# Kernel optimization log

Hardware: AMD Instinct MI355X
Metric: run time of the kernel (lower is better)

The kernel has to match this reference:

```python
import jax, jax.numpy as jnp
import numpy as np
import math

B, L, DF = 1024, 96, 5
D_MODEL, D_FF, N_HEADS = 256, 1024, 8
C_OUT, MA, FACTOR = 5, 25, 3
E_LAYERS, D_LAYERS, EXT = 2, 2, 20


def moving_mean(x, k):
    # torch moving_avg: replicate-pad (k-1)//2 on each side, AvgPool1d(k, stride=1)
    p = (k - 1) // 2
    xp = jnp.concatenate([jnp.repeat(x[:, :1], p, axis=1), x, jnp.repeat(x[:, -1:], p, axis=1)], axis=1)
    cs = jnp.cumsum(xp, axis=1)
    cs = jnp.concatenate([jnp.zeros_like(cs[:, :1]), cs], axis=1)
    return (cs[:, k:] - cs[:, :-k]) / k


def series_decomp(x, k):
    m = moving_mean(x, k)
    return x - m, m


def circ_conv3(x, W):
    # Conv1d(kernel=3, padding=1, padding_mode='circular', bias=False); x (B,T,C), W (O,C,3)
    xp = jnp.pad(x, ((0, 0), (1, 1), (0, 0)), mode='wrap')
    win = jnp.stack([xp[:, :-2], xp[:, 1:-1], xp[:, 2:]], axis=-1)  # (B,T,C,3)
    return jnp.einsum('btct,oct->bto'.replace('btct', 'blct').replace('bto', 'blo'), win, W)


def my_layernorm(x, g, b):
    # LayerNorm over last dim, then subtract per-(batch,channel) seasonal bias (mean over time)
    mu = x.mean(-1, keepdims=True)
    var = ((x - mu) ** 2).mean(-1, keepdims=True)
    xh = (x - mu) / jnp.sqrt(var + 1e-5) * g + b
    return xh - xh.mean(axis=1, keepdims=True)


def time_delay_agg(values, corr):
    # inference-mode time delay aggregation; values, corr: (B,H,E,Lv)
    Bv, H, E, Lv = values.shape
    top_k = int(FACTOR * math.log(Lv))
    mean_value = corr.mean(axis=(1, 2))              # (B,Lv)
    weights, delay = jax.lax.top_k(mean_value, top_k)  # (B,k)
    tmp_corr = jax.nn.softmax(weights, axis=-1)
    ar = jnp.arange(Lv)

    def body(acc, wd):
        w, d = wd                                    # (B,), (B,) int32
        idx = (ar[None, :] + d[:, None]) % Lv        # circular roll == gather on doubled values
        pattern = jnp.take_along_axis(values, idx[:, None, None, :], axis=-1)
        return acc + pattern * w[:, None, None, None], None

    acc, _ = jax.lax.scan(body, jnp.zeros_like(values), (tmp_corr.T, delay.T))
    return acc


def auto_correlation(q, k, v):
    # q (B,Lq,H,E); k,v (B,S,H,E)
    Bq, Lq, H, E = q.shape
    S = v.shape[1]
    if Lq > S:
        pad = jnp.zeros((Bq, Lq - S, H, E), q.dtype)
        k = jnp.concatenate([k, pad], axis=1)
        v = jnp.concatenate([v, pad], axis=1)
    else:
        k, v = k[:, :Lq], v[:, :Lq]
    qf = jnp.fft.rfft(q.transpose(0, 2, 3, 1), axis=-1)
    kf = jnp.fft.rfft(k.transpose(0, 2, 3, 1), axis=-1)
    corr = jnp.fft.irfft(qf * jnp.conj(kf), n=Lq, axis=-1)  # (B,H,E,Lq)
    V = time_delay_agg(v.transpose(0, 2, 3, 1), corr)
    return V.transpose(0, 3, 1, 2)


def ac_layer(xq, xkv, Wq, bq, Wk, bk, Wv, bv, Wo, bo):
    Bq, Lq, _ = xq.shape
    S = xkv.shape[1]
    q = (xq @ Wq.T + bq).reshape(Bq, Lq, N_HEADS, -1)
    k = (xkv @ Wk.T + bk).reshape(Bq, S, N_HEADS, -1)
    v = (xkv @ Wv.T + bv).reshape(Bq, S, N_HEADS, -1)
    V = auto_correlation(q, k, v).reshape(Bq, Lq, -1)
    return V @ Wo.T + bo


def setup_inputs() -> dict:
    ks = iter(jax.random.split(jax.random.key(0), 64))

    def rn(shape, s=0.05):
        return jax.random.normal(next(ks), shape, jnp.float32) * s

    dm, E, D = D_MODEL, E_LAYERS, D_LAYERS
    inp = {'x': jax.random.normal(next(ks), (B, L, DF), jnp.float32)}
    inp['we_enc'] = rn((dm, DF, 3), 0.3)
    inp['we_dec'] = rn((dm, DF, 3), 0.3)
    for w in ('Wq', 'Wk', 'Wv', 'Wo'):
        inp['enc_' + w] = rn((E, dm, dm))
        inp['enc_b' + w[1]] = rn((E, dm))
    inp['enc_W1'] = rn((E, D_FF, dm))
    inp['enc_W2'] = rn((E, dm, D_FF))
    inp['enc_ln_g'] = jnp.ones((dm,), jnp.float32)
    inp['enc_ln_b'] = jnp.zeros((dm,), jnp.float32)
    for p in ('s', 'c'):
        for w in ('Wq', 'Wk', 'Wv', 'Wo'):
            inp['dec_' + p + w] = rn((D, dm, dm))
            inp['dec_' + p + 'b' + w[1]] = rn((D, dm))
    inp['dec_W1'] = rn((D, D_FF, dm))
    inp['dec_W2'] = rn((D, dm, D_FF))
    inp['dec_Wt'] = rn((D, C_OUT, dm, 3), 0.3)
    inp['dec_ln_g'] = jnp.ones((dm,), jnp.float32)
    inp['dec_ln_b'] = jnp.zeros((dm,), jnp.float32)
    inp['proj_W'] = rn((C_OUT, dm), 0.3)
    inp['proj_b'] = jnp.zeros((C_OUT,), jnp.float32)
    inp['bn_g'] = jnp.ones((EXT,), jnp.float32)
    inp['bn_b'] = jnp.zeros((EXT,), jnp.float32)
    inp['bn_rm'] = jnp.zeros((EXT,), jnp.float32)
    inp['bn_rv'] = jnp.ones((EXT,), jnp.float32)
    inp['fc_W'] = rn((1, EXT), 0.3)
    inp['fc_b'] = jnp.zeros((1,), jnp.float32)
    return inp


def reference(x, we_enc, we_dec,
              enc_Wq, enc_bq, enc_Wk, enc_bk, enc_Wv, enc_bv, enc_Wo, enc_bo,
              enc_W1, enc_W2, enc_ln_g, enc_ln_b,
              dec_sWq, dec_sbq, dec_sWk, dec_sbk, dec_sWv, dec_sbv, dec_sWo, dec_sbo,
              dec_cWq, dec_cbq, dec_cWk, dec_cbk, dec_cWv, dec_cbv, dec_cWo, dec_cbo,
              dec_W1, dec_W2, dec_Wt, dec_ln_g, dec_ln_b,
              proj_W, proj_b, bn_g, bn_b, bn_rm, bn_rv, fc_W, fc_b):
    mean = jnp.tile(x.mean(axis=1, keepdims=True), (1, EXT, 1))
    seasonal_init, trend_init = series_decomp(x, MA)
    trend_init = jnp.concatenate([trend_init, mean], axis=1)            # (B, L+EXT, DF)
    seasonal_init = jnp.pad(seasonal_init, ((0, 0), (EXT, 0), (0, 0)))  # 20 zero steps in front
    # encoder
    enc = circ_conv3(x, we_enc)  # DataEmbedding_wo_pos (dropout = identity in eval)
    for i in range(E_LAYERS):
        a = ac_layer(enc, enc, enc_Wq[i], enc_bq[i], enc_Wk[i], enc_bk[i],
                     enc_Wv[i], enc_bv[i], enc_Wo[i], enc_bo[i])
        h, _ = series_decomp(enc + a, MA)
        y = jax.nn.relu(h @ enc_W1[i].T) @ enc_W2[i].T  # 1x1 convs, bias=False
        enc, _ = series_decomp(h + y, MA)
    enc = my_layernorm(enc, enc_ln_g, enc_ln_b)
    # decoder
    dec = circ_conv3(seasonal_init, we_dec)
    trend = trend_init
    for i in range(D_LAYERS):
        a = ac_layer(dec, dec, dec_sWq[i], dec_sbq[i], dec_sWk[i], dec_sbk[i],
                     dec_sWv[i], dec_sbv[i], dec_sWo[i], dec_sbo[i])
        dec, t1 = series_decomp(dec + a, MA)
        a = ac_layer(dec, enc, dec_cWq[i], dec_cbq[i], dec_cWk[i], dec_cbk[i],
                     dec_cWv[i], dec_cbv[i], dec_cWo[i], dec_cbo[i])
        dec, t2 = series_decomp(dec + a, MA)
        y = jax.nn.relu(dec @ dec_W1[i].T) @ dec_W2[i].T
        dec, t3 = series_decomp(dec + y, MA)
        trend = trend + circ_conv3(t1 + t2 + t3, dec_Wt[i])
    dec = my_layernorm(dec, dec_ln_g, dec_ln_b)
    seasonal = dec @ proj_W.T + proj_b          # (B, L+EXT, C_OUT)
    seasonal = jnp.tile(seasonal, (1, 1, 4))    # (B, L+EXT, 20)
    out = jnp.tile(trend, (1, 1, 4)) + seasonal  # trend tiled to 20 channels (see notes)
    last = out[:, -1, :]                         # (B, 20)
    h = (last - bn_rm) / jnp.sqrt(bn_rv + 1e-5) * bn_g + bn_b  # BatchNorm1d eval
    return (h @ fc_W.T + fc_b)[:, 0]
```

## Files before the change

### kernel.cpp

```cpp
#include <hip/hip_runtime.h>
#include <hip/hip_bf16.h>
#include <cstdint>
#include <cstddef>

#define B_   1024
#define LE   96
#define LD   116
#define DM   256
#define DFF  1024

typedef __attribute__((ext_vector_type(8))) short bf16x8;
typedef __attribute__((ext_vector_type(4))) float f32x4;

static __device__ __forceinline__ unsigned short f2b(float f) {
  __hip_bfloat16 h = __float2bfloat16(f);
  return *reinterpret_cast<unsigned short*>(&h);
}
static __device__ __forceinline__ float asf(unsigned int u) { return __uint_as_float(u); }

static __device__ __forceinline__ void split8(float4 a, float4 b, uint4& h4, uint4& l4) {
  float f[8] = {a.x, a.y, a.z, a.w, b.x, b.y, b.z, b.w};
  unsigned int hp[4], lp[4];
#pragma unroll
  for (int j = 0; j < 4; ++j) {
    unsigned short h0 = f2b(f[2 * j]);
    unsigned short h1 = f2b(f[2 * j + 1]);
    float r0 = f[2 * j]     - asf((unsigned int)h0 << 16);
    float r1 = f[2 * j + 1] - asf((unsigned int)h1 << 16);
    hp[j] = (unsigned int)h0 | ((unsigned int)h1 << 16);
    lp[j] = (unsigned int)f2b(r0) | ((unsigned int)f2b(r1) << 16);
  }
  h4 = make_uint4(hp[0], hp[1], hp[2], hp[3]);
  l4 = make_uint4(lp[0], lp[1], lp[2], lp[3]);
}

typedef const __attribute__((address_space(1))) void* gas_ptr;
typedef __attribute__((address_space(3))) void* las_ptr;
static __device__ __forceinline__ void gload16(const void* g, void* l) {
  __builtin_amdgcn_global_load_lds((gas_ptr)g, (las_ptr)l, 16, 0, 0);
}

#define NE_ ((size_t)B_ * LE * DM)
#define ND_ ((size_t)B_ * LD * DM)
#define NS_ ((size_t)B_ * LD * 5)
#define NW_ ((size_t)B_ * 16)
#define WBF_ 3670016

static constexpr size_t o_enc   = 0;
static constexpr size_t o_dec   = o_enc   + NE_ * 4;
static constexpr size_t o_q     = o_dec   + ND_ * 4;
static constexpr size_t o_kbuf  = o_q     + ND_ * 4;
static constexpr size_t o_qkv   = o_kbuf  + ND_ * 4;
static constexpr size_t o_spad  = o_qkv   + ND_ * 12;
static constexpr size_t o_trend = o_spad  + NS_ * 4;
static constexpr size_t o_wtop  = o_trend + NS_ * 4;
static constexpr size_t o_dtop  = o_wtop  + NW_ * 4;
static constexpr size_t o_bias  = o_dtop  + NW_ * 4;
static constexpr size_t o_whi   = o_bias  + 6 * 768 * 4;
static constexpr size_t o_wlo   = o_whi   + (size_t)WBF_ * 2;
static constexpr size_t WS_TOTAL = o_wlo  + (size_t)WBF_ * 2;

__device__ __align__(256) unsigned char g_ws[WS_TOTAL];

static __host__ __device__ constexpr size_t enc_base(int i) { return (size_t)i * 786432; }
static __host__ __device__ constexpr size_t dec_base(int i) { return 1572864 + (size_t)i * 1048576; }

__global__ __launch_bounds__(256)
void k_cast_split(const float* __restrict__ in, unsigned short* __restrict__ hi,
                  unsigned short* __restrict__ lo, int n) {
  int i = (blockIdx.x * 256 + threadIdx.x) * 4;
  if (i < n) {
    float4 v = *(const float4*)(in + i);
    unsigned int hp[2], lp[2];
    float f[4] = {v.x, v.y, v.z, v.w};
#pragma unroll
    for (int j = 0; j < 2; ++j) {
      unsigned short h0 = f2b(f[2 * j]);
      unsigned short h1 = f2b(f[2 * j + 1]);
      float r0 = f[2 * j]     - asf((unsigned int)h0 << 16);
      float r1 = f[2 * j + 1] - asf((unsigned int)h1 << 16);
      hp[j] = (unsigned int)h0 | ((unsigned int)h1 << 16);
      lp[j] = (unsigned int)f2b(r0) | ((unsigned int)f2b(r1) << 16);
    }
    *(uint2*)(hi + i) = make_uint2(hp[0], hp[1]);
    *(uint2*)(lo + i) = make_uint2(lp[0], lp[1]);
  }
}

__global__ __launch_bounds__(256)
void k_cat3(const float* __restrict__ a, const float* __restrict__ b,
            const float* __restrict__ c, float* __restrict__ dst) {
  int t = threadIdx.x;
  dst[t] = a[t];
  dst[256 + t] = b[t];
  if (c) dst[512 + t] = c[t];
}

__global__ __launch_bounds__(128)
void k_pre(const float* __restrict__ x, float* __restrict__ spad, float* __restrict__ trend) {
  int b = blockIdx.x;
  __shared__ float xs[LE * 5];
  __shared__ float mx[5];
  const float* xb = x + (size_t)b * LE * 5;
  for (int i = threadIdx.x; i < LE * 5; i += 128) xs[i] = xb[i];
  __syncthreads();
  if (threadIdx.x < 5) {
    float s = 0.f;
    for (int t = 0; t < LE; ++t) s += xs[t * 5 + threadIdx.x];
    mx[threadIdx.x] = s * (1.f / 96.f);
  }
  __syncthreads();
  float* spb = spad + (size_t)b * LD * 5;
  float* trb = trend + (size_t)b * LD * 5;
  for (int i = threadIdx.x; i < LE * 5; i += 128) {
    int t = i / 5, c = i % 5;
    float s = 0.f;
    for (int d = -12; d <= 12; ++d) {
      int tt = t + d; tt = tt < 0 ? 0 : (tt > LE - 1 ? LE - 1 : tt);
      s += xs[tt * 5 + c];
    }
    float m = s * (1.f / 25.f);
    trb[t * 5 + c] = m;
    spb[(t + 20) * 5 + c] = xs[i] - m;
  }
  for (int i = threadIdx.x; i < 20 * 5; i += 128) {
    int t = i / 5, c = i % 5;
    spb[t * 5 + c] = 0.f;
    trb[(LE + t) * 5 + c] = mx[c];
  }
}

__global__ __launch_bounds__(256)
void k_conv3(const float* __restrict__ xin, const float* __restrict__ W,
             float* __restrict__ out, int L) {
  int b = blockIdx.x, o = threadIdx.x;
  __shared__ float xs[LD * 5];
  const float* xb = xin + (size_t)b * L * 5;
  for (int i = o; i < L * 5; i += 256) xs[i] = xb[i];
  __syncthreads();
  float w[15];
#pragma unroll
  for (int j = 0; j < 15; ++j) w[j] = W[o * 15 + j];
  float* ob = out + (size_t)b * L * DM;
  for (int l = 0; l < L; ++l) {
    int lm = (l == 0) ? L - 1 : l - 1;
    int lp = (l == L - 1) ? 0 : l + 1;
    float acc = 0.f;
#pragma unroll
    for (int c = 0; c < 5; ++c)
      acc += xs[lm * 5 + c] * w[c * 3] + xs[l * 5 + c] * w[c * 3 + 1] + xs[lp * 5 + c] * w[c * 3 + 2];
    ob[(size_t)l * DM + o] = acc;
  }
}

template <bool RELU>
__global__ __launch_bounds__(256)
void k_gemm_split(const float* __restrict__ X,
                  const unsigned short* __restrict__ Whi, const unsigned short* __restrict__ Wlo,
                  const float* __restrict__ bias, float* __restrict__ C,
                  int M, int N, int K) {
  __shared__ __align__(16) unsigned short Xh[4096], Xl[4096], Wh[4096], Wl[4096];
  const int nwg = gridDim.x, bid = blockIdx.x;
  const int wg = (bid & 7) * (nwg >> 3) + (bid >> 3);
  const int NT = N >> 7;
  const int mt = wg / NT, nt = wg % NT;
  const int m0 = mt << 7, n0 = nt << 7;
  const int tid = threadIdx.x, lane = tid & 63, wv = tid >> 6;
  const int wm = (wv >> 1) << 6, wn = (wv & 1) << 6;

  f32x4 acc[4][4];
#pragma unroll
  for (int i = 0; i < 4; ++i)
#pragma unroll
    for (int j = 0; j < 4; ++j) acc[i][j] = (f32x4){0.f, 0.f, 0.f, 0.f};

  const int r0 = tid >> 2,        ls0 = (tid & 3) ^ ((r0 >> 1) & 3);
  const int r1 = 64 + (tid >> 2), ls1 = (tid & 3) ^ ((r1 >> 1) & 3);
  const unsigned short* wh0 = Whi + (size_t)(n0 + r0) * K + (ls0 << 3);
  const unsigned short* wh1 = Whi + (size_t)(n0 + r1) * K + (ls1 << 3);
  const unsigned short* wl0 = Wlo + (size_t)(n0 + r0) * K + (ls0 << 3);
  const unsigned short* wl1 = Wlo + (size_t)(n0 + r1) * K + (ls1 << 3);
  unsigned short* lwh0 = Wh + ((tid & ~63) << 3);
  unsigned short* lwh1 = Wh + 2048 + ((tid & ~63) << 3);
  unsigned short* lwl0 = Wl + ((tid & ~63) << 3);
  unsigned short* lwl1 = Wl + 2048 + ((tid & ~63) << 3);

  const int xrow0 = tid >> 2, xpart = tid & 3;
  const int xrow1 = 64 + xrow0;
  const float* xp0 = X + (size_t)(m0 + xrow0) * K + (xpart << 3);
  const float* xp1 = X + (size_t)(m0 + xrow1) * K + (xpart << 3);
  const int xph0 = xpart ^ ((xrow0 >> 1) & 3);
  const int xph1 = xpart ^ ((xrow1 >> 1) & 3);
  unsigned short* xh0d = Xh + xrow0 * 32 + (xph0 << 3);
  unsigned short* xl0d = Xl + xrow0 * 32 + (xph0 << 3);
  unsigned short* xh1d = Xh + xrow1 * 32 + (xph1 << 3);
  unsigned short* xl1d = Xl + xrow1 * 32 + (xph1 << 3);

  for (int k0 = 0; k0 < K; k0 += 32) {
    gload16(wh0 + k0, lwh0);
    gload16(wh1 + k0, lwh1);
    gload16(wl0 + k0, lwl0);
    gload16(wl1 + k0, lwl1);
    {
      float4 a0 = *(const float4*)(xp0 + k0);
      float4 b0 = *(const float4*)(xp0 + k0 + 4);
      float4 a1 = *(const float4*)(xp1 + k0);
      float4 b1 = *(const float4*)(xp1 + k0 + 4);
      uint4 h, l;
      split8(a0, b0, h, l);
      *(uint4*)xh0d = h; *(uint4*)xl0d = l;
      split8(a1, b1, h, l);
      *(uint4*)xh1d = h; *(uint4*)xl1d = l;
    }
    __syncthreads();
    bf16x8 ah[4], al[4], bh[4], bl[4];
#pragma unroll
    for (int i = 0; i < 4; ++i) {
      int ra = wm + i * 16 + (lane & 15);
      int sa = (lane >> 4) ^ ((ra >> 1) & 3);
      ah[i] = *(const bf16x8*)(Xh + ra * 32 + (sa << 3));
      al[i] = *(const bf16x8*)(Xl + ra * 32 + (sa << 3));
      int rb = wn + i * 16 + (lane & 15);
      int sb = (lane >> 4) ^ ((rb >> 1) & 3);
      bh[i] = *(const bf16x8*)(Wh + rb * 32 + (sb << 3));
      bl[i] = *(const bf16x8*)(Wl + rb * 32 + (sb << 3));
    }
#pragma unroll
    for (int i = 0; i < 4; ++i)
#pragma unroll
      for (int j = 0; j < 4; ++j) {
        acc[i][j] = __builtin_amdgcn_mfma_f32_16x16x32_bf16(ah[i], bh[j], acc[i][j], 0, 0, 0);
        acc[i][j] = __builtin_amdgcn_mfma_f32_16x16x32_bf16(al[i], bh[j], acc[i][j], 0, 0, 0);
        acc[i][j] = __builtin_amdgcn_mfma_f32_16x16x32_bf16(ah[i], bl[j], acc[i][j], 0, 0, 0);
      }
    __syncthreads();
  }

  const int col_base = n0 + wn + (lane & 15);
  const int row_base = m0 + wm + ((lane >> 4) << 2);
#pragma unroll
  for (int j = 0; j < 4; ++j) {
    int col = col_base + j * 16;
    float bv = bias ? bias[col] : 0.f;
#pragma unroll
    for (int i = 0; i < 4; ++i) {
      int rb2 = row_base + i * 16;
#pragma unroll
      for (int q = 0; q < 4; ++q) {
        float o = acc[i][j][q] + bv;
        if (RELU) o = fmaxf(o, 0.f);
        C[(size_t)(rb2 + q) * N + col] = o;
      }
    }
  }
}

__global__ __launch_bounds__(256)
void k_corr_split(const float* __restrict__ Q, int sq, const float* __restrict__ Kp, int sk,
                  float* __restrict__ wout, int* __restrict__ dout,
                  int L, int S, int TK) {
  __shared__ __align__(16) unsigned char smem[65536];
  unsigned short* qh = (unsigned short*)smem;
  unsigned short* ql = qh + 8192;
  unsigned short* kh = ql + 8192;
  unsigned short* kl = kh + 8192;
  float* G = (float*)smem;
  int b = blockIdx.x, tid = threadIdx.x, lane = tid & 63, wv = tid >> 6;
  int wm = (wv >> 1) << 6, wn = (wv & 1) << 6;
  const float* Qb = Q + (size_t)b * L * sq;
  const float* Kb = Kp + (size_t)b * S * sk;
  f32x4 acc[4][4];
#pragma unroll
  for (int i = 0; i < 4; ++i)
#pragma unroll
    for (int j = 0; j < 4; ++j) acc[i][j] = (f32x4){0.f, 0.f, 0.f, 0.f};

  for (int c0 = 0; c0 < DM; c0 += 64) {
#pragma unroll
    for (int u = 0; u < 4; ++u) {
      int seg = (u << 8) + tid;
      int row = seg >> 3, ps = seg & 7;
      int phys = ps ^ (row & 7);
      uint4 h = make_uint4(0u, 0u, 0u, 0u), l = make_uint4(0u, 0u, 0u, 0u);
      if (row < L) {
        float4 a = *(const float4*)(Qb + (size_t)row * sq + c0 + (ps << 3));
        float4 c = *(const float4*)(Qb + (size_t)row * sq + c0 + (ps << 3) + 4);
        split8(a, c, h, l);
      }
      *(uint4*)(qh + row * 64 + (phys << 3)) = h;
      *(uint4*)(ql + row * 64 + (phys << 3)) = l;
      h = make_uint4(0u, 0u, 0u, 0u); l = make_uint4(0u, 0u, 0u, 0u);
      if (row < S) {
        float4 a = *(const float4*)(Kb + (size_t)row * sk + c0 + (ps << 3));
        float4 c = *(const float4*)(Kb + (size_t)row * sk + c0 + (ps << 3) + 4);
        split8(a, c, h, l);
      }
      *(uint4*)(kh + row * 64 + (phys << 3)) = h;
      *(uint4*)(kl + row * 64 + (phys << 3)) = l;
    }
    __syncthreads();
#pragma unroll
    for (int ks = 0; ks < 2; ++ks) {
      bf16x8 aqh[4], aql[4], bkh[4], bkl[4];
#pragma unroll
      for (int i = 0; i < 4; ++i) {
        int ra = wm + i * 16 + (lane & 15);
        int sa = ((ks << 2) + (lane >> 4)) ^ (ra & 7);
        aqh[i] = *(const bf16x8*)(qh + ra * 64 + (sa << 3));
        aql[i] = *(const bf16x8*)(ql + ra * 64 + (sa << 3));
        int rb = wn + i * 16 + (lane & 15);
        int sb = ((ks << 2) + (lane >> 4)) ^ (rb & 7);
        bkh[i] = *(const bf16x8*)(kh + rb * 64 + (sb << 3));
        bkl[i] = *(const bf16x8*)(kl + rb * 64 + (sb << 3));
      }
#pragma unroll
      for (int i = 0; i < 4; ++i)
#pragma unroll
        for (int j = 0; j < 4; ++j) {
          acc[i][j] = __builtin_amdgcn_mfma_f32_16x16x32_bf16(aqh[i], bkh[j], acc[i][j], 0, 0, 0);
          acc[i][j] = __builtin_amdgcn_mfma_f32_16x16x32_bf16(aql[i], bkh[j], acc[i][j], 0, 0, 0);
          acc[i][j] = __builtin_amdgcn_mfma_f32_16x16x32_bf16(aqh[i], bkl[j], acc[i][j], 0, 0, 0);
        }
    }
    __syncthreads();
  }
#pragma unroll
  for (int i = 0; i < 4; ++i)
#pragma unroll
    for (int j = 0; j < 4; ++j)
#pragma unroll
      for (int q = 0; q < 4; ++q)
        G[(wm + i * 16 + ((lane >> 4) << 2) + q) * 128 + wn + j * 16 + (lane & 15)] = acc[i][j][q];
  __syncthreads();
  float s = 0.f;
  if (tid < L) {
    for (int t = 0; t < L; ++t) {
      int r = t - tid; if (r < 0) r += L;
      s += G[t * 128 + r];
    }
    s *= (1.f / 256.f);
  }
  __syncthreads();

  float* vals = (float*)smem;
  float* rv   = vals + 128;
  int*   ri   = (int*)(rv + 128);
  float* selv = (float*)(ri + 128);
  int*   seli = (int*)(selv + 16);
  if (tid < 128) vals[tid] = (tid < L) ? s : -3e38f;
  __syncthreads();
  for (int it = 0; it < TK; ++it) {
    if (tid < 128) { rv[tid] = vals[tid]; ri[tid] = tid; }
    __syncthreads();
    for (int off = 64; off >= 1; off >>= 1) {
      if (tid < off) {
        float v2 = rv[tid + off]; int i2 = ri[tid + off];
        if (v2 > rv[tid] || (v2 == rv[tid] && i2 < ri[tid])) { rv[tid] = v2; ri[tid] = i2; }
      }
      __syncthreads();
    }
    if (tid == 0) { selv[it] = rv[0]; seli[it] = ri[0]; vals[ri[0]] = -3e38f; }
    __syncthreads();
  }
  if (tid == 0) {
    float mxv = selv[0];
    float e[16]; float sum = 0.f;
    for (int j = 0; j < TK; ++j) { e[j] = expf(selv[j] - mxv); sum += e[j]; }
    float inv = 1.f / sum;
    for (int j = 0; j < TK; ++j) {
      wout[(size_t)b * 16 + j] = e[j] * inv;
      dout[(size_t)b * 16 + j] = seli[j];
    }
  }
}

__global__ __launch_bounds__(256)
void k_gather4(const float* __restrict__ V, int sv, const float* __restrict__ wtop,
               const int* __restrict__ dtop, float* __restrict__ out,
               int L, int S, int TK, int G8) {
  int p = blockIdx.x;
  int xcd = p & 7, q8 = p >> 3;
  int lg = q8 % G8;
  int b = ((q8 / G8) << 3) + xcd;
  __shared__ float wsm[16];
  __shared__ int   dsm[16];
  if (threadIdx.x < TK) {
    wsm[threadIdx.x] = wtop[(size_t)b * 16 + threadIdx.x];
    dsm[threadIdx.x] = dtop[(size_t)b * 16 + threadIdx.x];
  }
  __syncthreads();
  int wv = threadIdx.x >> 6, lane = threadIdx.x & 63;
  int c4 = lane << 2;
  const float* Vb = V + (size_t)b * S * sv + c4;
  float* ob = out + (size_t)b * L * DM + c4;
#pragma unroll
  for (int u = 0; u < 2; ++u) {
    int l = (lg << 3) + (wv << 1) + u;
    if (l < L) {
      float ax = 0.f, ay = 0.f, az = 0.f, aw = 0.f;
      for (int j = 0; j < TK; ++j) {
        int r = l + dsm[j]; if (r >= L) r -= L;
        if (r < S) {
          float4 v = *(const float4*)(Vb + (size_t)r * sv);
          float w = wsm[j];
          ax += w * v.x; ay += w * v.y; az += w * v.z; aw += w * v.w;
        }
      }
      float4 o; o.x = ax; o.y = ay; o.z = az; o.w = aw;
      *(float4*)(ob + (size_t)l * DM) = o;
    }
  }
}

template <int MOUT>
__global__ __launch_bounds__(128)
void k_decomp(const float* __restrict__ X, const float* __restrict__ Y,
              float* __restrict__ out, float* __restrict__ mout, int L) {
  int b = blockIdx.x >> 2, qd = blockIdx.x & 3;
  __shared__ float tmp[LD * 64];
  size_t base = (size_t)b * L * DM + qd * 64;
  for (int i = threadIdx.x; i < L * 64; i += 128) {
    int t = i >> 6, cc = i & 63;
    size_t gi = base + (size_t)t * DM + cc;
    tmp[i] = X[gi] + Y[gi];
  }
  __syncthreads();
  int c = threadIdx.x & 63, th = threadIdx.x >> 6;
  int half = L >> 1;
  int t0 = th * half, t1 = t0 + half;
  float s = 0.f;
  for (int d = -12; d <= 12; ++d) {
    int t2 = t0 + d; t2 = t2 < 0 ? 0 : (t2 > L - 1 ? L - 1 : t2);
    s += tmp[t2 * 64 + c];
  }
  for (int t = t0; t < t1; ++t) {
    float m = s * (1.f / 25.f);
    size_t gi = base + (size_t)t * DM + c;
    out[gi] = tmp[t * 64 + c] - m;
    if (MOUT) mout[gi] = m;
    int ai = t + 13; if (ai > L - 1) ai = L - 1;
    int si = t - 12; if (si < 0) si = 0;
    s += tmp[ai * 64 + c] - tmp[si * 64 + c];
  }
}

__global__ __launch_bounds__(256)
void k_lnorm(const float* __restrict__ X, const float* __restrict__ g,
             float* __restrict__ out, int L) {
  int b = blockIdx.x;
  __shared__ float mu_s[LD], inv_s[LD];
  size_t base = (size_t)b * L * DM;
  int wv = threadIdx.x >> 6, lane = threadIdx.x & 63;
  for (int t = wv; t < L; t += 4) {
    float s = 0.f, s2 = 0.f;
#pragma unroll
    for (int qd = 0; qd < 4; ++qd) {
      float val = X[base + (size_t)t * DM + lane + 64 * qd];
      s += val; s2 += val * val;
    }
    for (int off = 32; off; off >>= 1) { s += __shfl_xor(s, off); s2 += __shfl_xor(s2, off); }
    if (lane == 0) {
      float mu = s * (1.f / 256.f);
      mu_s[t] = mu;
      inv_s[t] = rsqrtf(s2 * (1.f / 256.f) - mu * mu + 1e-5f);
    }
  }
  __syncthreads();
  int c = threadIdx.x;
  float gc = g[c];
  float sm = 0.f;
  for (int t = 0; t < L; ++t) sm += (X[base + (size_t)t * DM + c] - mu_s[t]) * inv_s[t];
  float mn = sm / (float)L;
  for (int t = 0; t < L; ++t) {
    float xn = (X[base + (size_t)t * DM + c] - mu_s[t]) * inv_s[t];
    out[base + (size_t)t * DM + c] = gc * (xn - mn);
  }
}

__global__ __launch_bounds__(256)
void k_trendconv(const float* __restrict__ T, const float* __restrict__ Wt,
                 float* __restrict__ trend, int L) {
  int b = blockIdx.x;
  int tid = threadIdx.x, wv = tid >> 6, lane = tid & 63;
  int c0 = lane << 2;
  float w[5][3][4];
#pragma unroll
  for (int o = 0; o < 5; ++o)
#pragma unroll
    for (int k = 0; k < 4; ++k) {
      w[o][0][k] = Wt[o * 768 + (c0 + k) * 3 + 0];
      w[o][1][k] = Wt[o * 768 + (c0 + k) * 3 + 1];
      w[o][2][k] = Wt[o * 768 + (c0 + k) * 3 + 2];
    }
  size_t base = (size_t)b * L * DM;
  for (int l = wv; l < L; l += 4) {
    int lm = (l == 0) ? L - 1 : l - 1;
    int lp = (l == L - 1) ? 0 : l + 1;
    float4 xm = *(const float4*)(T + base + (size_t)lm * DM + c0);
    float4 x0 = *(const float4*)(T + base + (size_t)l  * DM + c0);
    float4 xp = *(const float4*)(T + base + (size_t)lp * DM + c0);
    float fm[4] = {xm.x, xm.y, xm.z, xm.w};
    float f0[4] = {x0.x, x0.y, x0.z, x0.w};
    float fp[4] = {xp.x, xp.y, xp.z, xp.w};
    float acc[5];
#pragma unroll
    for (int o = 0; o < 5; ++o) {
      float a = 0.f;
#pragma unroll
      for (int k = 0; k < 4; ++k)
        a += fm[k] * w[o][0][k] + f0[k] * w[o][1][k] + fp[k] * w[o][2][k];
      acc[o] = a;
    }
#pragma unroll
    for (int off = 32; off; off >>= 1)
#pragma unroll
      for (int o = 0; o < 5; ++o) acc[o] += __shfl_xor(acc[o], off);
    if (lane == 0) {
#pragma unroll
      for (int o = 0; o < 5; ++o)
        trend[((size_t)b * L + l) * 5 + o] += acc[o];
    }
  }
}

__global__ __launch_bounds__(256)
void k_final(const float* __restrict__ dec, const float* __restrict__ trend,
             const float* __restrict__ projW, const float* __restrict__ projb,
             const float* __restrict__ bng, const float* __restrict__ bnb,
             const float* __restrict__ bnrm, const float* __restrict__ bnrv,
             const float* __restrict__ fcW, const float* __restrict__ fcb,
             float* __restrict__ outp) {
  int b = blockIdx.x, c = threadIdx.x;
  __shared__ float red[5][256];
  float xv = dec[((size_t)b * LD + (LD - 1)) * DM + c];
#pragma unroll
  for (int o = 0; o < 5; ++o) red[o][c] = xv * projW[o * 256 + c];
  __syncthreads();
  for (int off = 128; off >= 1; off >>= 1) {
    if (c < off) {
#pragma unroll
      for (int o = 0; o < 5; ++o) red[o][c] += red[o][c + off];
    }
    __syncthreads();
  }
  if (c == 0) {
    float acc = fcb[0];
    for (int j = 0; j < 20; ++j) {
      int m5 = j % 5;
      float last = trend[((size_t)b * LD + (LD - 1)) * 5 + m5] + red[m5][0] + projb[m5];
      float h = (last - bnrm[j]) * rsqrtf(bnrv[j] + 1e-5f) * bng[j] + bnb[j];
      acc += h * fcW[j];
    }
    outp[b] = acc;
  }
}

extern "C" void kernel_launch(void* const* d_in, const int* in_sizes, int n_in,
                              void* d_out, int out_size, void* d_ws, size_t ws_size,
                              hipStream_t stream) {
  const float* x      = (const float*)d_in[0];
  const float* we_enc = (const float*)d_in[1];
  const float* we_dec = (const float*)d_in[2];
  const float* enc_Wq = (const float*)d_in[3];
  const float* enc_bq = (const float*)d_in[4];
  const float* enc_Wk = (const float*)d_in[5];
  const float* enc_bk = (const float*)d_in[6];
  const float* enc_Wv = (const float*)d_in[7];
  const float* enc_bv = (const float*)d_in[8];
  const float* enc_Wo = (const float*)d_in[9];
  const float* enc_bo = (const float*)d_in[10];
  const float* enc_W1 = (const float*)d_in[11];
  const float* enc_W2 = (const float*)d_in[12];
  const float* enc_g  = (const float*)d_in[13];
  const float* sWq = (const float*)d_in[15]; const float* sbq = (const float*)d_in[16];
  const float* sWk = (const float*)d_in[17]; const float* sbk = (const float*)d_in[18];
  const float* sWv = (const float*)d_in[19]; const float* sbv = (const float*)d_in[20];
  const float* sWo = (const float*)d_in[21]; const float* sbo = (const float*)d_in[22];
  const float* cWq = (const float*)d_in[23]; const float* cbq = (const float*)d_in[24];
  const float* cWk = (const float*)d_in[25]; const float* cbk = (const float*)d_in[26];
  const float* cWv = (const float*)d_in[27]; const float* cbv = (const float*)d_in[28];
  const float* cWo = (const float*)d_in[29]; const float* cbo = (const float*)d_in[30];
  const float* dW1 = (const float*)d_in[31]; const float* dW2 = (const float*)d_in[32];
  const float* dWt = (const float*)d_in[33];
  const float* dec_g  = (const float*)d_in[34];
  const float* projW = (const float*)d_in[36]; const float* projb = (const float*)d_in[37];
  const float* bng = (const float*)d_in[38]; const float* bnb = (const float*)d_in[39];
  const float* bnrm = (const float*)d_in[40]; const float* bnrv = (const float*)d_in[41];
  const float* fcW = (const float*)d_in[42]; const float* fcb = (const float*)d_in[43];
  (void)in_sizes; (void)n_in; (void)out_size; (void)d_ws; (void)ws_size;
  float* outp = (float*)d_out;

  void* symaddr = nullptr;
  if (hipGetSymbolAddress(&symaddr, HIP_SYMBOL(g_ws)) != hipSuccess || !symaddr) return;
  unsigned char* base = (unsigned char*)symaddr;
  float* enc   = (float*)(base + o_enc);
  float* dec   = (float*)(base + o_dec);
  float* q     = (float*)(base + o_q);
  float* kbuf  = (float*)(base + o_kbuf);
  float* qkv   = (float*)(base + o_qkv);
  float* spad  = (float*)(base + o_spad);
  float* trend = (float*)(base + o_trend);
  float* wtop  = (float*)(base + o_wtop);
  int*   dtop  = (int*)(base + o_dtop);
  float* biasb = (float*)(base + o_bias);
  unsigned short* whi = (unsigned short*)(base + o_whi);
  unsigned short* wlo = (unsigned short*)(base + o_wlo);

  const int ME = B_ * LE;
  const int MD = B_ * LD;

  auto cast = [&](const float* s, size_t off, int n) {
    k_cast_split<<<n / 1024, 256, 0, stream>>>(s, whi + off, wlo + off, n);
  };
  for (int i = 0; i < 2; ++i) {
    size_t e = enc_base(i), d = dec_base(i);
    size_t wq = (size_t)i * 65536, wf = (size_t)i * 262144;
    cast(enc_Wq + wq, e + 0, 65536);       cast(enc_Wk + wq, e + 65536, 65536);
    cast(enc_Wv + wq, e + 131072, 65536);  cast(enc_Wo + wq, e + 196608, 65536);
    cast(enc_W1 + wf, e + 262144, 262144); cast(enc_W2 + wf, e + 524288, 262144);
    cast(sWq + wq, d + 0, 65536);          cast(sWk + wq, d + 65536, 65536);
    cast(sWv + wq, d + 131072, 65536);     cast(sWo + wq, d + 196608, 65536);
    cast(cWq + wq, d + 262144, 65536);     cast(cWk + wq, d + 327680, 65536);
    cast(cWv + wq, d + 393216, 65536);     cast(cWo + wq, d + 458752, 65536);
    cast(dW1 + wf, d + 524288, 262144);    cast(dW2 + wf, d + 786432, 262144);
    size_t b_ = (size_t)i * DM;
    k_cat3<<<1, 256, 0, stream>>>(enc_bq + b_, enc_bk + b_, enc_bv + b_, biasb + (size_t)i * 768);
    k_cat3<<<1, 256, 0, stream>>>(sbq + b_, sbk + b_, sbv + b_, biasb + (size_t)(2 + i) * 768);
    k_cat3<<<1, 256, 0, stream>>>(cbk + b_, cbv + b_, nullptr, biasb + (size_t)(4 + i) * 768);
  }

  auto gemm = [&](const float* X, size_t woff, const float* bias, float* C,
                  int M, int N, int K, bool relu) {
    int nwg = (M >> 7) * (N >> 7);
    if (relu) k_gemm_split<true ><<<nwg, 256, 0, stream>>>(X, whi + woff, wlo + woff, bias, C, M, N, K);
    else      k_gemm_split<false><<<nwg, 256, 0, stream>>>(X, whi + woff, wlo + woff, bias, C, M, N, K);
  };
  auto ffn = [&](const float* xb, int M, size_t w1, size_t w2) {
    int done = 0;
    while (done < M) {
      int mc = (M - done < 29696) ? (M - done) : 29696;
      gemm(xb + (size_t)done * DM, w1, nullptr, q, mc, DFF, DM, true);
      gemm(q, w2, nullptr, kbuf + (size_t)done * DM, mc, DM, DFF, false);
      done += mc;
    }
  };
  auto attn_self = [&](const float* src, int Lq, size_t wqkv, size_t wo2,
                       const float* biasr, const float* bo, int TK) {
    int M = B_ * Lq;
    int G8 = (Lq + 7) >> 3;
    gemm(src, wqkv, biasr, qkv, M, 768, DM, false);
    k_corr_split<<<B_, 256, 0, stream>>>(qkv, 768, qkv + 256, 768, wtop, dtop, Lq, Lq, TK);
    k_gather4<<<B_ * G8, 256, 0, stream>>>(qkv + 512, 768, wtop, dtop, kbuf, Lq, Lq, TK, G8);
    gemm(kbuf, wo2, bo, q, M, DM, DM, false);
  };
  auto attn_cross = [&](size_t wq2, size_t wkv, size_t wo2, const float* bq,
                        const float* biasr, const float* bo, int TK) {
    int G8 = (LD + 7) >> 3;
    gemm(dec, wq2, bq, q, MD, DM, DM, false);
    gemm(enc, wkv, biasr, qkv, ME, 512, DM, false);
    k_corr_split<<<B_, 256, 0, stream>>>(q, 256, qkv, 512, wtop, dtop, LD, LE, TK);
    k_gather4<<<B_ * G8, 256, 0, stream>>>(qkv + 256, 512, wtop, dtop, kbuf, LD, LE, TK, G8);
    gemm(kbuf, wo2, bo, q, MD, DM, DM, false);
  };

  k_pre<<<B_, 128, 0, stream>>>(x, spad, trend);
  k_conv3<<<B_, 256, 0, stream>>>(x, we_enc, enc, LE);
  k_conv3<<<B_, 256, 0, stream>>>(spad, we_dec, dec, LD);

  for (int i = 0; i < 2; ++i) {
    size_t e = enc_base(i), b_ = (size_t)i * DM;
    attn_self(enc, LE, e + 0, e + 196608, biasb + (size_t)i * 768, enc_bo + b_, 13);
    k_decomp<0><<<4 * B_, 128, 0, stream>>>(enc, q, enc, nullptr, LE);
    ffn(enc, ME, e + 262144, e + 524288);
    k_decomp<0><<<4 * B_, 128, 0, stream>>>(enc, kbuf, enc, nullptr, LE);
  }
  k_lnorm<<<B_, 256, 0, stream>>>(enc, enc_g, enc, LE);

  for (int i = 0; i < 2; ++i) {
    size_t d = dec_base(i), b_ = (size_t)i * DM;
    const float* Wt_i = dWt + (size_t)i * 5 * DM * 3;
    attn_self(dec, LD, d + 0, d + 196608, biasb + (size_t)(2 + i) * 768, sbo + b_, 14);
    k_decomp<1><<<4 * B_, 128, 0, stream>>>(dec, q, dec, kbuf, LD);
    k_trendconv<<<B_, 256, 0, stream>>>(kbuf, Wt_i, trend, LD);
    attn_cross(d + 262144, d + 327680, d + 458752, cbq + b_, biasb + (size_t)(4 + i) * 768, cbo + b_, 14);
    k_decomp<1><<<4 * B_, 128, 0, stream>>>(dec, q, dec, kbuf, LD);
    k_trendconv<<<B_, 256, 0, stream>>>(kbuf, Wt_i, trend, LD);
    ffn(dec, MD, d + 524288, d + 786432);
    k_decomp<1><<<4 * B_, 128, 0, stream>>>(dec, kbuf, dec, q, LD);
    k_trendconv<<<B_, 256, 0, stream>>>(q, Wt_i, trend, LD);
  }
  k_lnorm<<<B_, 256, 0, stream>>>(dec, dec_g, dec, LD);

  k_final<<<B_, 256, 0, stream>>>(dec, trend, projW, projb, bng, bnb, bnrm, bnrv, fcW, fcb, outp);
}
```

Before: 6.296 ms.

## Emit pre-split bf16 hi/lo activations from producers; GEMM loads both via LDS DMA

Every kernel that produces a GEMM input (conv3, decomp, layernorm, gather, FFN first GEMM) now also writes bf16 hi/lo split copies of its activations. The GEMM then loads X through global_load_lds, the same way it loads weights, instead of loading fp32 and splitting in registers. This takes the per-tile conversion and the register-to-LDS stores out of the GEMM inner loop, and the FFN hidden layer becomes half-width bf16 pairs instead of fp32. The cost is extra write traffic from the elementwise producers and a larger workspace.

```diff
diff --git a/kernel.cpp b/kernel.cpp
--- a/kernel.cpp
+++ b/kernel.cpp
@@ -17,18 +17,21 @@
   return *reinterpret_cast<unsigned short*>(&h);
 }
 static __device__ __forceinline__ float asf(unsigned int u) { return __uint_as_float(u); }
+static __device__ __forceinline__ void split1(float f, unsigned short& h, unsigned short& l) {
+  h = f2b(f);
+  l = f2b(f - asf((unsigned int)h << 16));
+}
 
 static __device__ __forceinline__ void split8(float4 a, float4 b, uint4& h4, uint4& l4) {
   float f[8] = {a.x, a.y, a.z, a.w, b.x, b.y, b.z, b.w};
   unsigned int hp[4], lp[4];
 #pragma unroll
   for (int j = 0; j < 4; ++j) {
-    unsigned short h0 = f2b(f[2 * j]);
-    unsigned short h1 = f2b(f[2 * j + 1]);
-    float r0 = f[2 * j]     - asf((unsigned int)h0 << 16);
-    float r1 = f[2 * j + 1] - asf((unsigned int)h1 << 16);
+    unsigned short h0, l0, h1, l1;
+    split1(f[2 * j], h0, l0);
+    split1(f[2 * j + 1], h1, l1);
     hp[j] = (unsigned int)h0 | ((unsigned int)h1 << 16);
-    lp[j] = (unsigned int)f2b(r0) | ((unsigned int)f2b(r1) << 16);
+    lp[j] = (unsigned int)l0 | ((unsigned int)l1 << 16);
   }
   h4 = make_uint4(hp[0], hp[1], hp[2], hp[3]);
   l4 = make_uint4(lp[0], lp[1], lp[2], lp[3]);
@@ -44,6 +47,7 @@
 #define ND_ ((size_t)B_ * LD * DM)
 #define NS_ ((size_t)B_ * LD * 5)
 #define NW_ ((size_t)B_ * 16)
+#define HID_ ((size_t)29696 * DFF)
 #define WBF_ 3670016
 
 static constexpr size_t o_enc   = 0;
@@ -51,7 +55,15 @@
 static constexpr size_t o_q     = o_dec   + ND_ * 4;
 static constexpr size_t o_kbuf  = o_q     + ND_ * 4;
 static constexpr size_t o_qkv   = o_kbuf  + ND_ * 4;
-static constexpr size_t o_spad  = o_qkv   + ND_ * 12;
+static constexpr size_t o_ench  = o_qkv   + ND_ * 12;
+static constexpr size_t o_encl  = o_ench  + NE_ * 2;
+static constexpr size_t o_dech  = o_encl  + NE_ * 2;
+static constexpr size_t o_decl  = o_dech  + ND_ * 2;
+static constexpr size_t o_gthh  = o_decl  + ND_ * 2;
+static constexpr size_t o_gthl  = o_gthh  + ND_ * 2;
+static constexpr size_t o_hidh  = o_gthl  + ND_ * 2;
+static constexpr size_t o_hidl  = o_hidh  + HID_ * 2;
+static constexpr size_t o_spad  = o_hidl  + HID_ * 2;
 static constexpr size_t o_trend = o_spad  + NS_ * 4;
 static constexpr size_t o_wtop  = o_trend + NS_ * 4;
 static constexpr size_t o_dtop  = o_wtop  + NW_ * 4;
@@ -75,12 +87,11 @@
     float f[4] = {v.x, v.y, v.z, v.w};
 #pragma unroll
     for (int j = 0; j < 2; ++j) {
-      unsigned short h0 = f2b(f[2 * j]);
-      unsigned short h1 = f2b(f[2 * j + 1]);
-      float r0 = f[2 * j]     - asf((unsigned int)h0 << 16);
-      float r1 = f[2 * j + 1] - asf((unsigned int)h1 << 16);
+      unsigned short h0, l0, h1, l1;
+      split1(f[2 * j], h0, l0);
+      split1(f[2 * j + 1], h1, l1);
       hp[j] = (unsigned int)h0 | ((unsigned int)h1 << 16);
-      lp[j] = (unsigned int)f2b(r0) | ((unsigned int)f2b(r1) << 16);
+      lp[j] = (unsigned int)l0 | ((unsigned int)l1 << 16);
     }
     *(uint2*)(hi + i) = make_uint2(hp[0], hp[1]);
     *(uint2*)(lo + i) = make_uint2(lp[0], lp[1]);
@@ -132,7 +143,8 @@
 
 __global__ __launch_bounds__(256)
 void k_conv3(const float* __restrict__ xin, const float* __restrict__ W,
-             float* __restrict__ out, int L) {
+             float* __restrict__ out, unsigned short* __restrict__ ohi,
+             unsigned short* __restrict__ olo, int L) {
   int b = blockIdx.x, o = threadIdx.x;
   __shared__ float xs[LD * 5];
   const float* xb = xin + (size_t)b * L * 5;
@@ -141,7 +153,7 @@
   float w[15];
 #pragma unroll
   for (int j = 0; j < 15; ++j) w[j] = W[o * 15 + j];
-  float* ob = out + (size_t)b * L * DM;
+  size_t ob = (size_t)b * L * DM + o;
   for (int l = 0; l < L; ++l) {
     int lm = (l == 0) ? L - 1 : l - 1;
     int lp = (l == L - 1) ? 0 : l + 1;
@@ -149,16 +161,20 @@
 #pragma unroll
     for (int c = 0; c < 5; ++c)
       acc += xs[lm * 5 + c] * w[c * 3] + xs[l * 5 + c] * w[c * 3 + 1] + xs[lp * 5 + c] * w[c * 3 + 2];
-    ob[(size_t)l * DM + o] = acc;
-  }
-}
-
-template <bool RELU>
-__global__ __launch_bounds__(256)
-void k_gemm_split(const float* __restrict__ X,
-                  const unsigned short* __restrict__ Whi, const unsigned short* __restrict__ Wlo,
-                  const float* __restrict__ bias, float* __restrict__ C,
-                  int M, int N, int K) {
+    size_t gi = ob + (size_t)l * DM;
+    out[gi] = acc;
+    unsigned short h, lo2; split1(acc, h, lo2);
+    ohi[gi] = h; olo[gi] = lo2;
+  }
+}
+
+template <int OMODE, bool RELU>
+__global__ __launch_bounds__(256)
+void k_gemm_ps(const unsigned short* __restrict__ Xhi, const unsigned short* __restrict__ Xlo,
+               const unsigned short* __restrict__ Whi, const unsigned short* __restrict__ Wlo,
+               const float* __restrict__ bias, float* __restrict__ Cf,
+               unsigned short* __restrict__ Chi, unsigned short* __restrict__ Clo,
+               int M, int N, int K) {
   __shared__ __align__(16) unsigned short Xh[4096], Xl[4096], Wh[4096], Wl[4096];
   const int nwg = gridDim.x, bid = blockIdx.x;
   const int wg = (bid & 7) * (nwg >> 3) + (bid >> 3);
@@ -176,42 +192,25 @@
 
   const int r0 = tid >> 2,        ls0 = (tid & 3) ^ ((r0 >> 1) & 3);
   const int r1 = 64 + (tid >> 2), ls1 = (tid & 3) ^ ((r1 >> 1) & 3);
+  const unsigned short* xh0 = Xhi + (size_t)(m0 + r0) * K + (ls0 << 3);
+  const unsigned short* xh1 = Xhi + (size_t)(m0 + r1) * K + (ls1 << 3);
+  const unsigned short* xl0 = Xlo + (size_t)(m0 + r0) * K + (ls0 << 3);
+  const unsigned short* xl1 = Xlo + (size_t)(m0 + r1) * K + (ls1 << 3);
   const unsigned short* wh0 = Whi + (size_t)(n0 + r0) * K + (ls0 << 3);
   const unsigned short* wh1 = Whi + (size_t)(n0 + r1) * K + (ls1 << 3);
   const unsigned short* wl0 = Wlo + (size_t)(n0 + r0) * K + (ls0 << 3);
   const unsigned short* wl1 = Wlo + (size_t)(n0 + r1) * K + (ls1 << 3);
-  unsigned short* lwh0 = Wh + ((tid & ~63) << 3);
-  unsigned short* lwh1 = Wh + 2048 + ((tid & ~63) << 3);
-  unsigned short* lwl0 = Wl + ((tid & ~63) << 3);
-  unsigned short* lwl1 = Wl + 2048 + ((tid & ~63) << 3);
-
-  const int xrow0 = tid >> 2, xpart = tid & 3;
-  const int xrow1 = 64 + xrow0;
-  const float* xp0 = X + (size_t)(m0 + xrow0) * K + (xpart << 3);
-  const float* xp1 = X + (size_t)(m0 + xrow1) * K + (xpart << 3);
-  const int xph0 = xpart ^ ((xrow0 >> 1) & 3);
-  const int xph1 = xpart ^ ((xrow1 >> 1) & 3);
-  unsigned short* xh0d = Xh + xrow0 * 32 + (xph0 << 3);
-  unsigned short* xl0d = Xl + xrow0 * 32 + (xph0 << 3);
-  unsigned short* xh1d = Xh + xrow1 * 32 + (xph1 << 3);
-  unsigned short* xl1d = Xl + xrow1 * 32 + (xph1 << 3);
+  const int lofs0 = (tid & ~63) << 3, lofs1 = 2048 + ((tid & ~63) << 3);
 
   for (int k0 = 0; k0 < K; k0 += 32) {
-    gload16(wh0 + k0, lwh0);
-    gload16(wh1 + k0, lwh1);
-    gload16(wl0 + k0, lwl0);
-    gload16(wl1 + k0, lwl1);
-    {
-      float4 a0 = *(const float4*)(xp0 + k0);
-      float4 b0 = *(const float4*)(xp0 + k0 + 4);
-      float4 a1 = *(const float4*)(xp1 + k0);
-      float4 b1 = *(const float4*)(xp1 + k0 + 4);
-      uint4 h, l;
-      split8(a0, b0, h, l);
-      *(uint4*)xh0d = h; *(uint4*)xl0d = l;
-      split8(a1, b1, h, l);
-      *(uint4*)xh1d = h; *(uint4*)xl1d = l;
-    }
+    gload16(xh0 + k0, Xh + lofs0);
+    gload16(xh1 + k0, Xh + lofs1);
+    gload16(xl0 + k0, Xl + lofs0);
+    gload16(xl1 + k0, Xl + lofs1);
+    gload16(wh0 + k0, Wh + lofs0);
+    gload16(wh1 + k0, Wh + lofs1);
+    gload16(wl0 + k0, Wl + lofs0);
+    gload16(wl1 + k0, Wl + lofs1);
     __syncthreads();
     bf16x8 ah[4], al[4], bh[4], bl[4];
 #pragma unroll
@@ -249,7 +248,13 @@
       for (int q = 0; q < 4; ++q) {
         float o = acc[i][j][q] + bv;
         if (RELU) o = fmaxf(o, 0.f);
-        C[(size_t)(rb2 + q) * N + col] = o;
+        size_t idx = (size_t)(rb2 + q) * N + col;
+        if (OMODE == 0) {
+          Cf[idx] = o;
+        } else {
+          unsigned short h, l; split1(o, h, l);
+          Chi[idx] = h; Clo[idx] = l;
+        }
       }
     }
   }
@@ -376,8 +381,8 @@
 
 __global__ __launch_bounds__(256)
 void k_gather4(const float* __restrict__ V, int sv, const float* __restrict__ wtop,
-               const int* __restrict__ dtop, float* __restrict__ out,
-               int L, int S, int TK, int G8) {
+               const int* __restrict__ dtop, unsigned short* __restrict__ ohi,
+               unsigned short* __restrict__ olo, int L, int S, int TK, int G8) {
   int p = blockIdx.x;
   int xcd = p & 7, q8 = p >> 3;
   int lg = q8 % G8;
@@ -392,22 +397,29 @@
   int wv = threadIdx.x >> 6, lane = threadIdx.x & 63;
   int c4 = lane << 2;
   const float* Vb = V + (size_t)b * S * sv + c4;
-  float* ob = out + (size_t)b * L * DM + c4;
+  size_t ob = (size_t)b * L * DM + c4;
 #pragma unroll
   for (int u = 0; u < 2; ++u) {
     int l = (lg << 3) + (wv << 1) + u;
     if (l < L) {
-      float ax = 0.f, ay = 0.f, az = 0.f, aw = 0.f;
+      float a0 = 0.f, a1 = 0.f, a2 = 0.f, a3 = 0.f;
       for (int j = 0; j < TK; ++j) {
         int r = l + dsm[j]; if (r >= L) r -= L;
         if (r < S) {
           float4 v = *(const float4*)(Vb + (size_t)r * sv);
           float w = wsm[j];
-          ax += w * v.x; ay += w * v.y; az += w * v.z; aw += w * v.w;
+          a0 += w * v.x; a1 += w * v.y; a2 += w * v.z; a3 += w * v.w;
         }
       }
-      float4 o; o.x = ax; o.y = ay; o.z = az; o.w = aw;
-      *(float4*)(ob + (size_t)l * DM) = o;
+      unsigned short h0, l0, h1, l1, h2, l2, h3, l3;
+      split1(a0, h0, l0); split1(a1, h1, l1); split1(a2, h2, l2); split1(a3, h3, l3);
+      uint2 hp, lp;
+      hp.x = (unsigned int)h0 | ((unsigned int)h1 << 16);
+      hp.y = (unsigned int)h2 | ((unsigned int)h3 << 16);
+      lp.x = (unsigned int)l0 | ((unsigned int)l1 << 16);
+      lp.y = (unsigned int)l2 | ((unsigned int)l3 << 16);
+      *(uint2*)(ohi + ob + (size_t)l * DM) = hp;
+      *(uint2*)(olo + ob + (size_t)l * DM) = lp;
     }
   }
 }
@@ -415,7 +427,8 @@
 template <int MOUT>
 __global__ __launch_bounds__(128)
 void k_decomp(const float* __restrict__ X, const float* __restrict__ Y,
-              float* __restrict__ out, float* __restrict__ mout, int L) {
+              float* __restrict__ out, unsigned short* __restrict__ ohi,
+              unsigned short* __restrict__ olo, float* __restrict__ mout, int L) {
   int b = blockIdx.x >> 2, qd = blockIdx.x & 3;
   __shared__ float tmp[LD * 64];
   size_t base = (size_t)b * L * DM + qd * 64;
@@ -436,7 +449,10 @@
   for (int t = t0; t < t1; ++t) {
     float m = s * (1.f / 25.f);
     size_t gi = base + (size_t)t * DM + c;
-    out[gi] = tmp[t * 64 + c] - m;
+    float o = tmp[t * 64 + c] - m;
+    out[gi] = o;
+    unsigned short h, l; split1(o, h, l);
+    ohi[gi] = h; olo[gi] = l;
     if (MOUT) mout[gi] = m;
     int ai = t + 13; if (ai > L - 1) ai = L - 1;
     int si = t - 12; if (si < 0) si = 0;
@@ -446,7 +462,8 @@
 
 __global__ __launch_bounds__(256)
 void k_lnorm(const float* __restrict__ X, const float* __restrict__ g,
-             float* __restrict__ out, int L) {
+             float* __restrict__ out, unsigned short* __restrict__ ohi,
+             unsigned short* __restrict__ olo, int L) {
   int b = blockIdx.x;
   __shared__ float mu_s[LD], inv_s[LD];
   size_t base = (size_t)b * L * DM;
@@ -473,7 +490,11 @@
   float mn = sm / (float)L;
   for (int t = 0; t < L; ++t) {
     float xn = (X[base + (size_t)t * DM + c] - mu_s[t]) * inv_s[t];
-    out[base + (size_t)t * DM + c] = gc * (xn - mn);
+    float o = gc * (xn - mn);
+    size_t gi = base + (size_t)t * DM + c;
+    out[gi] = o;
+    unsigned short h, l; split1(o, h, l);
+    ohi[gi] = h; olo[gi] = l;
   }
 }
 
@@ -598,6 +619,14 @@
   float* q     = (float*)(base + o_q);
   float* kbuf  = (float*)(base + o_kbuf);
   float* qkv   = (float*)(base + o_qkv);
+  unsigned short* ench = (unsigned short*)(base + o_ench);
+  unsigned short* encl = (unsigned short*)(base + o_encl);
+  unsigned short* dech = (unsigned short*)(base + o_dech);
+  unsigned short* decl = (unsigned short*)(base + o_decl);
+  unsigned short* gthh = (unsigned short*)(base + o_gthh);
+  unsigned short* gthl = (unsigned short*)(base + o_gthl);
+  unsigned short* hidh = (unsigned short*)(base + o_hidh);
+  unsigned short* hidl = (unsigned short*)(base + o_hidl);
   float* spad  = (float*)(base + o_spad);
   float* trend = (float*)(base + o_trend);
   float* wtop  = (float*)(base + o_wtop);
@@ -629,67 +658,74 @@
     k_cat3<<<1, 256, 0, stream>>>(cbk + b_, cbv + b_, nullptr, biasb + (size_t)(4 + i) * 768);
   }
 
-  auto gemm = [&](const float* X, size_t woff, const float* bias, float* C,
-                  int M, int N, int K, bool relu) {
+  auto gemm_f = [&](const unsigned short* Xh, const unsigned short* Xl, size_t woff,
+                    const float* bias, float* Cf, int M, int N, int K) {
     int nwg = (M >> 7) * (N >> 7);
-    if (relu) k_gemm_split<true ><<<nwg, 256, 0, stream>>>(X, whi + woff, wlo + woff, bias, C, M, N, K);
-    else      k_gemm_split<false><<<nwg, 256, 0, stream>>>(X, whi + woff, wlo + woff, bias, C, M, N, K);
+    k_gemm_ps<0, false><<<nwg, 256, 0, stream>>>(Xh, Xl, whi + woff, wlo + woff, bias,
+                                                 Cf, nullptr, nullptr, M, N, K);
   };
-  auto ffn = [&](const float* xb, int M, size_t w1, size_t w2) {
+  auto gemm_hl_relu = [&](const unsigned short* Xh, const unsigned short* Xl, size_t woff,
+                          unsigned short* Ch, unsigned short* Cl, int M, int N, int K) {
+    int nwg = (M >> 7) * (N >> 7);
+    k_gemm_ps<1, true><<<nwg, 256, 0, stream>>>(Xh, Xl, whi + woff, wlo + woff, nullptr,
+                                                nullptr, Ch, Cl, M, N, K);
+  };
+  auto ffn = [&](const unsigned short* srch, const unsigned short* srcl, int M,
+                 size_t w1, size_t w2) {
     int done = 0;
     while (done < M) {
       int mc = (M - done < 29696) ? (M - done) : 29696;
-      gemm(xb + (size_t)done * DM, w1, nullptr, q, mc, DFF, DM, true);
-      gemm(q, w2, nullptr, kbuf + (size_t)done * DM, mc, DM, DFF, false);
+      gemm_hl_relu(srch + (size_t)done * DM, srcl + (size_t)done * DM, w1, hidh, hidl, mc, DFF, DM);
+      gemm_f(hidh, hidl, w2, nullptr, kbuf + (size_t)done * DM, mc, DM, DFF);
       done += mc;
     }
   };
-  auto attn_self = [&](const float* src, int Lq, size_t wqkv, size_t wo2,
-                       const float* biasr, const float* bo, int TK) {
+  auto attn_self = [&](const unsigned short* srch, const unsigned short* srcl, int Lq,
+                       size_t wqkv, size_t wo2, const float* biasr, const float* bo, int TK) {
     int M = B_ * Lq;
     int G8 = (Lq + 7) >> 3;
-    gemm(src, wqkv, biasr, qkv, M, 768, DM, false);
+    gemm_f(srch, srcl, wqkv, biasr, qkv, M, 768, DM);
     k_corr_split<<<B_, 256, 0, stream>>>(qkv, 768, qkv + 256, 768, wtop, dtop, Lq, Lq, TK);
-    k_gather4<<<B_ * G8, 256, 0, stream>>>(qkv + 512, 768, wtop, dtop, kbuf, Lq, Lq, TK, G8);
-    gemm(kbuf, wo2, bo, q, M, DM, DM, false);
+    k_gather4<<<B_ * G8, 256, 0, stream>>>(qkv + 512, 768, wtop, dtop, gthh, gthl, Lq, Lq, TK, G8);
+    gemm_f(gthh, gthl, wo2, bo, q, M, DM, DM);
   };
   auto attn_cross = [&](size_t wq2, size_t wkv, size_t wo2, const float* bq,
                         const float* biasr, const float* bo, int TK) {
     int G8 = (LD + 7) >> 3;
-    gemm(dec, wq2, bq, q, MD, DM, DM, false);
-    gemm(enc, wkv, biasr, qkv, ME, 512, DM, false);
+    gemm_f(dech, decl, wq2, bq, q, MD, DM, DM);
+    gemm_f(ench, encl, wkv, biasr, qkv, ME, 512, DM);
     k_corr_split<<<B_, 256, 0, stream>>>(q, 256, qkv, 512, wtop, dtop, LD, LE, TK);
-    k_gather4<<<B_ * G8, 256, 0, stream>>>(qkv + 256, 512, wtop, dtop, kbuf, LD, LE, TK, G8);
-    gemm(kbuf, wo2, bo, q, MD, DM, DM, false);
+    k_gather4<<<B_ * G8, 256, 0, stream>>>(qkv + 256, 512, wtop, dtop, gthh, gthl, LD, LE, TK, G8);
+    gemm_f(gthh, gthl, wo2, bo, q, MD, DM, DM);
   };
 
   k_pre<<<B_, 128, 0, stream>>>(x, spad, trend);
-  k_conv3<<<B_, 256, 0, stream>>>(x, we_enc, enc, LE);
-  k_conv3<<<B_, 256, 0, stream>>>(spad, we_dec, dec, LD);
+  k_conv3<<<B_, 256, 0, stream>>>(x, we_enc, enc, ench, encl, LE);
+  k_conv3<<<B_, 256, 0, stream>>>(spad, we_dec, dec, dech, decl, LD);
 
   for (int i = 0; i < 2; ++i) {
     size_t e = enc_base(i), b_ = (size_t)i * DM;
-    attn_self(enc, LE, e + 0, e + 196608, biasb + (size_t)i * 768, enc_bo + b_, 13);
-    k_decomp<0><<<4 * B_, 128, 0, stream>>>(enc, q, enc, nullptr, LE);
-    ffn(enc, ME, e + 262144, e + 524288);
-    k_decomp<0><<<4 * B_, 128, 0, stream>>>(enc, kbuf, enc, nullptr, LE);
-  }
-  k_lnorm<<<B_, 256, 0, stream>>>(enc, enc_g, enc, LE);
+    attn_self(ench, encl, LE, e + 0, e + 196608, biasb + (size_t)i * 768, enc_bo + b_, 13);
+    k_decomp<0><<<4 * B_, 128, 0, stream>>>(enc, q, enc, ench, encl, nullptr, LE);
+    ffn(ench, encl, ME, e + 262144, e + 524288);
+    k_decomp<0><<<4 * B_, 128, 0, stream>>>(enc, kbuf, enc, ench, encl, nullptr, LE);
+  }
+  k_lnorm<<<B_, 256, 0, stream>>>(enc, enc_g, enc, ench, encl, LE);
 
   for (int i = 0; i < 2; ++i) {
     size_t d = dec_base(i), b_ = (size_t)i * DM;
     const float* Wt_i = dWt + (size_t)i * 5 * DM * 3;
-    attn_self(dec, LD, d + 0, d + 196608, biasb + (size_t)(2 + i) * 768, sbo + b_, 14);
-    k_decomp<1><<<4 * B_, 128, 0, stream>>>(dec, q, dec, kbuf, LD);
+    attn_self(dech, decl, LD, d + 0, d + 196608, biasb + (size_t)(2 + i) * 768, sbo + b_, 14);
+    k_decomp<1><<<4 * B_, 128, 0, stream>>>(dec, q, dec, dech, decl, kbuf, LD);
     k_trendconv<<<B_, 256, 0, stream>>>(kbuf, Wt_i, trend, LD);
     attn_cross(d + 262144, d + 327680, d + 458752, cbq + b_, biasb + (size_t)(4 + i) * 768, cbo + b_, 14);
-    k_decomp<1><<<4 * B_, 128, 0, stream>>>(dec, q, dec, kbuf, LD);
+    k_decomp<1><<<4 * B_, 128, 0, stream>>>(dec, q, dec, dech, decl, kbuf, LD);
     k_trendconv<<<B_, 256, 0, stream>>>(kbuf, Wt_i, trend, LD);
-    ffn(dec, MD, d + 524288, d + 786432);
-    k_decomp<1><<<4 * B_, 128, 0, stream>>>(dec, kbuf, dec, q, LD);
+    ffn(dech, decl, MD, d + 524288, d + 786432);
+    k_decomp<1><<<4 * B_, 128, 0, stream>>>(dec, kbuf, dec, dech, decl, q, LD);
     k_trendconv<<<B_, 256, 0, stream>>>(q, Wt_i, trend, LD);
   }
-  k_lnorm<<<B_, 256, 0, stream>>>(dec, dec_g, dec, LD);
+  k_lnorm<<<B_, 256, 0, stream>>>(dec, dec_g, dec, dech, decl, LD);
 
   k_final<<<B_, 256, 0, stream>>>(dec, trend, projW, projb, bng, bnb, bnrm, bnrv, fcW, fcb, outp);
 }
```

Result: slower. 6.682 ms (+6.1%).
